# Optimization experiments

Measured on AMD Instinct MI355X. Metric: run time of the kernel, lower is better.

Reference implementation:

```python
import jax, jax.numpy as jnp
import numpy as np

N_NODES = 20000
N_GRAPH = 256
NODE_DIM = 128
MULS = (128, 64, 32)       # node irreps: 128x0e + 64x1o + 32x2e
HC = 32                    # hidden channels per irrep
HIDDEN_DIM = 64
N_PATH = 9                 # feasible uuw paths into 0e+1e+2e
W_NUMEL = N_PATH * HC * HC # 9216


def _tables():
    # real Clebsch-Gordan tensors built from cartesian tensor algebra,
    # normalized so that sum(C**2) = 2*l_out + 1 (component normalization)
    eps = np.zeros((3, 3, 3))
    eps[0, 1, 2] = eps[1, 2, 0] = eps[2, 0, 1] = 1.0
    eps[0, 2, 1] = eps[2, 1, 0] = eps[1, 0, 2] = -1.0
    s2, s6 = 1 / np.sqrt(2), 1 / np.sqrt(6)
    Q2 = np.zeros((5, 3, 3))  # orthonormal basis of traceless symmetric 3x3
    Q2[0, 0, 1] = Q2[0, 1, 0] = s2          # xy
    Q2[1, 1, 2] = Q2[1, 2, 1] = s2          # yz
    Q2[2, 0, 0] = Q2[2, 1, 1] = -s6; Q2[2, 2, 2] = 2 * s6  # z2
    Q2[3, 0, 2] = Q2[3, 2, 0] = s2          # xz
    Q2[4, 0, 0] = s2; Q2[4, 1, 1] = -s2     # x2-y2

    def nrm(C, l3):
        return C * np.sqrt((2 * l3 + 1) / (C ** 2).sum())

    C000 = np.ones((1, 1, 1))
    C022 = np.eye(5)[None, :, :]
    C110 = np.eye(3).reshape(3, 3, 1) / np.sqrt(3)
    C111 = eps / np.sqrt(2)
    C112 = np.transpose(Q2, (1, 2, 0))
    C202 = np.eye(5)[:, None, :]
    C220 = np.eye(5).reshape(5, 5, 1) / np.sqrt(5)
    M = np.einsum('iab,jdb->ijad', Q2, Q2)  # [5,5,3,3]
    C221 = nrm(np.einsum('cad,ijad->ijc', eps, M), 1)
    S = 0.5 * (M + np.transpose(M, (0, 1, 3, 2)))
    S = S - np.trace(S, axis1=2, axis2=3)[..., None, None] * np.eye(3) / 3.0
    C222 = nrm(np.einsum('kad,ijad->ijk', Q2, S), 2)
    # sph2cart change of basis: 9 spherical comps (0e+1e+2e) -> 3x3 cartesian
    Qc = np.zeros((3, 3, 9))
    Qc[:, :, 0] = np.eye(3) / np.sqrt(3)        # isotropic part
    Qc[:, :, 1:4] = eps / np.sqrt(2)            # antisymmetric part
    Qc[:, :, 4:9] = np.transpose(Q2, (1, 2, 0)) # symmetric traceless part
    return [C000, C022, C110, C111, C112, C202, C220, C221, C222], Qc

_CGS, _QC = _tables()


def setup_inputs() -> dict:
    key = jax.random.key(0)
    ks = jax.random.split(key, 12)
    f32 = jnp.float32
    d_sph = MULS[0] + 3 * MULS[1] + 5 * MULS[2]  # 480
    return {
        'x_scalar': jax.random.normal(ks[0], (N_NODES, NODE_DIM), f32),
        'x_spherical': jax.random.normal(ks[1], (N_NODES, d_sph), f32),
        'batch': jnp.sort(jax.random.randint(ks[2], (N_NODES,), 0, N_GRAPH)),
        'W0e': jax.random.normal(ks[3], (MULS[0], HC), f32),
        'W1o': jax.random.normal(ks[4], (MULS[1], HC), f32),
        'W2e': jax.random.normal(ks[5], (MULS[2], HC), f32),
        'Wm1': jax.random.normal(ks[6], (NODE_DIM, HIDDEN_DIM), f32) / np.sqrt(NODE_DIM),
        'bm1': jnp.zeros((HIDDEN_DIM,), f32),
        'Wm2': jax.random.normal(ks[7], (HIDDEN_DIM, W_NUMEL), f32) / np.sqrt(HIDDEN_DIM),
        'bm2': jnp.zeros((W_NUMEL,), f32),
        'P0': jax.random.normal(ks[8], (3 * HC,), f32),
        'P1': jax.random.normal(ks[9], (2 * HC,), f32),
        'P2': jax.random.normal(ks[10], (4 * HC,), f32),
    }


def reference(x_scalar, x_spherical, batch, W0e, W1o, W2e, Wm1, bm1, Wm2, bm2, P0, P1, P2):
    n = x_scalar.shape[0]
    m0, m1, m2 = MULS
    # split node features into irrep blocks
    x0 = x_spherical[:, :m0, None]                        # [N,128,1] 0e
    x1 = x_spherical[:, m0:m0 + 3 * m1].reshape(n, m1, 3) # [N,64,3]  1o
    x2 = x_spherical[:, m0 + 3 * m1:].reshape(n, m2, 5)   # [N,32,5]  2e
    # pre_lin: per-irrep channel mixing (e3nn-style 1/sqrt(fan_in))
    h = [jnp.einsum('num,uv->nvm', x, W) / np.sqrt(W.shape[0])
         for x, W in ((x0, W0e), (x1, W1o), (x2, W2e))]   # each [N,32,2l+1]
    # per-node tensor-product weights from scalar features
    w = (jax.nn.silu(x_scalar @ Wm1 + bm1) @ Wm2 + bm2).reshape(n, N_PATH, HC, HC)
    # uuw tensor product, path order matches _CGS
    paths = ((0, 0), (0, 2), (1, 1), (1, 1), (1, 1), (2, 0), (2, 2), (2, 2), (2, 2))
    inv_u = 1.0 / np.sqrt(HC)
    outs = []
    for k, (i, j) in enumerate(paths):
        C = jnp.asarray(_CGS[k], x_scalar.dtype)
        outs.append(jnp.einsum('pqr,nup,nuq,nuw->nwr', C, h[i], h[j], w[:, k]) * inv_u)
    # post_lin: combine paths of each output l into a single channel
    y0 = jnp.einsum('num,u->nm', jnp.concatenate([outs[0], outs[2], outs[6]], 1), P0) / np.sqrt(3 * HC)
    y1 = jnp.einsum('num,u->nm', jnp.concatenate([outs[3], outs[7]], 1), P1) / np.sqrt(2 * HC)
    y2 = jnp.einsum('num,u->nm', jnp.concatenate([outs[1], outs[4], outs[5], outs[8]], 1), P2) / np.sqrt(4 * HC)
    sph = jnp.concatenate([y0, y1, y2], axis=1)           # [N,9]
    cart = jnp.einsum('abi,ni->nab', jnp.asarray(_QC, sph.dtype), sph)  # [N,3,3]
    red = jax.ops.segment_sum(cart, batch, num_segments=N_GRAPH)        # [B,3,3]
    # if_trace is False (if_iso=False): roll every non-batch dim by 1
    return jnp.roll(jnp.roll(red, 1, axis=1), 1, axis=2)
```

## Files before the change

kernel.cpp:

```cpp
#include <hip/hip_runtime.h>
#include <math.h>

#define OFF_W2P 0
#define OFF_B2P 12288
#define WS_FLOATS 12480

#define SC_Y0 0.0180421959121758f
#define SC_Y2 0.015625f
#define S2f 0.70710678118654752f
#define S6f 0.40824829046386302f
#define TWOS2f 1.41421356237309505f
#define TWOS6f 0.81649658092772603f
#define ISQRT3 0.57735026918962576f
#define ISQRT5 0.44721359549995794f
#define H0SC 0.08838834764831845f
#define H1SC 0.125f
#define H2SC 0.17677669529663689f

__device__ static inline float dot32(const float* __restrict__ a,
                                     const float* __restrict__ b) {
  const float4* a4 = (const float4*)a;
  const float4* b4 = (const float4*)b;
  float acc = 0.f;
#pragma unroll
  for (int q = 0; q < 8; ++q) {
    float4 x = a4[q], y = b4[q];
    acc += x.x * y.x + x.y * y.y + x.z * y.z + x.w * y.w;
  }
  return acc;
}

__global__ __launch_bounds__(256) void prep_kernel(
    const float* __restrict__ Wm2, const float* __restrict__ bm2,
    const float* __restrict__ P0, const float* __restrict__ P2,
    float* __restrict__ ws, float* __restrict__ out) {
  int j = blockIdx.x * 256 + threadIdx.x;
  if (j < 2304) out[j] = 0.f;

  if (j < 12288) {
    const int c = j / 192, o = j % 192;
    const int s = o >> 5, u = o & 31;
    int k; const float* P; float sc;
    switch (s) {
      case 0: k = 0; P = P0;      sc = SC_Y0; break;
      case 1: k = 1; P = P2;      sc = SC_Y2; break;
      case 2: k = 2; P = P0 + 32; sc = SC_Y0; break;
      case 3: k = 4; P = P2 + 32; sc = SC_Y2; break;
      case 4: k = 6; P = P0 + 64; sc = SC_Y0; break;
      default: k = 8; P = P2 + 96; sc = SC_Y2; break;
    }
    float acc = dot32(Wm2 + c * 9216 + k * 1024 + u * 32, P);
    if (s == 1) acc += dot32(Wm2 + c * 9216 + 5 * 1024 + u * 32, P2 + 64);
    ws[OFF_W2P + j] = acc * sc;
  } else if (j < 12480) {
    const int o = j - 12288;
    const int s = o >> 5, u = o & 31;
    int k; const float* P; float sc;
    switch (s) {
      case 0: k = 0; P = P0;      sc = SC_Y0; break;
      case 1: k = 1; P = P2;      sc = SC_Y2; break;
      case 2: k = 2; P = P0 + 32; sc = SC_Y0; break;
      case 3: k = 4; P = P2 + 32; sc = SC_Y2; break;
      case 4: k = 6; P = P0 + 64; sc = SC_Y0; break;
      default: k = 8; P = P2 + 96; sc = SC_Y2; break;
    }
    float acc = dot32(bm2 + k * 1024 + u * 32, P);
    if (s == 1) acc += dot32(bm2 + 5 * 1024 + u * 32, P2 + 64);
    ws[OFF_B2P + o] = acc * sc;
  }
}

__global__ __launch_bounds__(256, 4) void fused_kernel(
    const float* __restrict__ xs_g, const float* __restrict__ xsph,
    const float* __restrict__ W0e, const float* __restrict__ W1o,
    const float* __restrict__ W2e,
    const float* __restrict__ Wm1, const float* __restrict__ bm1,
    const float* __restrict__ ws, const int* __restrict__ batch,
    float* __restrict__ out, const float norm2) {
  __shared__ __align__(16) float smem[9312];
  float (*xp)[512] = (float (*)[512])smem;
  float (*Vt)[192] = (float (*)[192])smem;
  float (*hi2)[64] = (float (*)[64])(smem + 8192);
  float (*sphs)[6] = (float (*)[6])(smem + 9216);

  const int tid = threadIdx.x;
  const int n0 = blockIdx.x * 16;

  float4 st[7];
  float4 st7;
#pragma unroll
  for (int k = 0; k < 7; ++k) {
    const int d = tid + k * 256;
    const int r = d / 120, c = d % 120;
    st[k] = *(const float4*)(xsph + (size_t)(n0 + r) * 480 + c * 4);
  }
  if (tid < 128) {
    const int d = tid + 1792;
    const int r = d / 120, c = d % 120;
    st7 = *(const float4*)(xsph + (size_t)(n0 + r) * 480 + c * 4);
  }

  {
    const int n = tid >> 4, c0 = (tid & 15) * 4;
    const float* xr = xs_g + (size_t)(n0 + n) * 128;
    float a0 = 0.f, a1 = 0.f, a2 = 0.f, a3 = 0.f;
#pragma unroll 4
    for (int mq = 0; mq < 32; ++mq) {
      const float4 xv = *(const float4*)(xr + mq * 4);
      const float4 w0 = *(const float4*)(Wm1 + (mq * 4 + 0) * 64 + c0);
      const float4 w1 = *(const float4*)(Wm1 + (mq * 4 + 1) * 64 + c0);
      const float4 w2 = *(const float4*)(Wm1 + (mq * 4 + 2) * 64 + c0);
      const float4 w3 = *(const float4*)(Wm1 + (mq * 4 + 3) * 64 + c0);
      a0 += xv.x * w0.x + xv.y * w1.x + xv.z * w2.x + xv.w * w3.x;
      a1 += xv.x * w0.y + xv.y * w1.y + xv.z * w2.y + xv.w * w3.y;
      a2 += xv.x * w0.z + xv.y * w1.z + xv.z * w2.z + xv.w * w3.z;
      a3 += xv.x * w0.w + xv.y * w1.w + xv.z * w2.w + xv.w * w3.w;
    }
    const float4 bb = *(const float4*)(bm1 + c0);
    const float z0 = a0 + bb.x, z1 = a1 + bb.y, z2 = a2 + bb.z, z3 = a3 + bb.w;
    float4 s;
    s.x = z0 / (1.f + __expf(-z0));
    s.y = z1 / (1.f + __expf(-z1));
    s.z = z2 / (1.f + __expf(-z2));
    s.w = z3 / (1.f + __expf(-z3));
    *(float4*)&hi2[n][c0] = s;
  }

#pragma unroll
  for (int k = 0; k < 7; ++k) {
    const int d = tid + k * 256;
    const int r = d / 120, c = d % 120;
    *(float4*)&xp[r][c * 4] = st[k];
  }
  if (tid < 128) {
    const int d = tid + 1792;
    const int r = d / 120, c = d % 120;
    *(float4*)&xp[r][c * 4] = st7;
  }
  __syncthreads();

  const int u = tid & 31, ni = tid >> 5;
  const float* rowA = xp[ni];
  const float* rowB = xp[ni + 8];

  float h0A, h0B;
  {
    float aA = 0.f, aB = 0.f;
#pragma unroll 4
    for (int mq = 0; mq < 32; ++mq) {
      const float4 xa = *(const float4*)(rowA + mq * 4);
      const float4 xb = *(const float4*)(rowB + mq * 4);
      const float w0 = W0e[(mq * 4 + 0) * 32 + u];
      const float w1 = W0e[(mq * 4 + 1) * 32 + u];
      const float w2 = W0e[(mq * 4 + 2) * 32 + u];
      const float w3 = W0e[(mq * 4 + 3) * 32 + u];
      aA += xa.x * w0 + xa.y * w1 + xa.z * w2 + xa.w * w3;
      aB += xb.x * w0 + xb.y * w1 + xb.z * w2 + xb.w * w3;
    }
    h0A = aA * H0SC; h0B = aB * H0SC;
  }

  float h1A[3], h1B[3];
  {
    float aA[3] = {0.f, 0.f, 0.f}, aB[3] = {0.f, 0.f, 0.f};
#pragma unroll 2
    for (int mq = 0; mq < 16; ++mq) {
      const float4 a0 = *(const float4*)(rowA + 128 + mq * 12);
      const float4 a1 = *(const float4*)(rowA + 128 + mq * 12 + 4);
      const float4 a2 = *(const float4*)(rowA + 128 + mq * 12 + 8);
      const float4 b0 = *(const float4*)(rowB + 128 + mq * 12);
      const float4 b1 = *(const float4*)(rowB + 128 + mq * 12 + 4);
      const float4 b2 = *(const float4*)(rowB + 128 + mq * 12 + 8);
      const float xa[12] = {a0.x, a0.y, a0.z, a0.w, a1.x, a1.y, a1.z, a1.w,
                            a2.x, a2.y, a2.z, a2.w};
      const float xb[12] = {b0.x, b0.y, b0.z, b0.w, b1.x, b1.y, b1.z, b1.w,
                            b2.x, b2.y, b2.z, b2.w};
#pragma unroll
      for (int mm = 0; mm < 4; ++mm) {
        const float w = W1o[(mq * 4 + mm) * 32 + u];
#pragma unroll
        for (int j = 0; j < 3; ++j) {
          aA[j] += xa[mm * 3 + j] * w;
          aB[j] += xb[mm * 3 + j] * w;
        }
      }
    }
#pragma unroll
    for (int j = 0; j < 3; ++j) { h1A[j] = aA[j] * H1SC; h1B[j] = aB[j] * H1SC; }
  }

  float h2A[5], h2B[5];
  {
    float aA[5] = {0.f, 0.f, 0.f, 0.f, 0.f}, aB[5] = {0.f, 0.f, 0.f, 0.f, 0.f};
#pragma unroll 2
    for (int mq = 0; mq < 8; ++mq) {
      const float4 a0 = *(const float4*)(rowA + 320 + mq * 20);
      const float4 a1 = *(const float4*)(rowA + 320 + mq * 20 + 4);
      const float4 a2 = *(const float4*)(rowA + 320 + mq * 20 + 8);
      const float4 a3 = *(const float4*)(rowA + 320 + mq * 20 + 12);
      const float4 a4 = *(const float4*)(rowA + 320 + mq * 20 + 16);
      const float4 b0 = *(const float4*)(rowB + 320 + mq * 20);
      const float4 b1 = *(const float4*)(rowB + 320 + mq * 20 + 4);
      const float4 b2 = *(const float4*)(rowB + 320 + mq * 20 + 8);
      const float4 b3 = *(const float4*)(rowB + 320 + mq * 20 + 12);
      const float4 b4 = *(const float4*)(rowB + 320 + mq * 20 + 16);
      const float xa[20] = {a0.x, a0.y, a0.z, a0.w, a1.x, a1.y, a1.z, a1.w,
                            a2.x, a2.y, a2.z, a2.w, a3.x, a3.y, a3.z, a3.w,
                            a4.x, a4.y, a4.z, a4.w};
      const float xb[20] = {b0.x, b0.y, b0.z, b0.w, b1.x, b1.y, b1.z, b1.w,
                            b2.x, b2.y, b2.z, b2.w, b3.x, b3.y, b3.z, b3.w,
                            b4.x, b4.y, b4.z, b4.w};
#pragma unroll
      for (int mm = 0; mm < 4; ++mm) {
        const float w = W2e[(mq * 4 + mm) * 32 + u];
#pragma unroll
        for (int j = 0; j < 5; ++j) {
          aA[j] += xa[mm * 5 + j] * w;
          aB[j] += xb[mm * 5 + j] * w;
        }
      }
    }
#pragma unroll
    for (int j = 0; j < 5; ++j) { h2A[j] = aA[j] * H2SC; h2B[j] = aB[j] * H2SC; }
  }
  __syncthreads();

  if (tid < 192) {
    const int o = tid;
    float acc[16];
    {
      const float b = ws[OFF_B2P + o];
#pragma unroll
      for (int n = 0; n < 16; ++n) acc[n] = b;
    }
    for (int c4 = 0; c4 < 64; c4 += 4) {
      const float w0 = ws[OFF_W2P + (c4 + 0) * 192 + o];
      const float w1 = ws[OFF_W2P + (c4 + 1) * 192 + o];
      const float w2 = ws[OFF_W2P + (c4 + 2) * 192 + o];
      const float w3 = ws[OFF_W2P + (c4 + 3) * 192 + o];
#pragma unroll
      for (int n = 0; n < 16; ++n) {
        const float4 h = *(const float4*)&hi2[n][c4];
        acc[n] += h.x * w0 + h.y * w1 + h.z * w2 + h.w * w3;
      }
    }
#pragma unroll
    for (int n = 0; n < 16; ++n) Vt[n][o] = acc[n];
  }
  __syncthreads();

#pragma unroll
  for (int it = 0; it < 2; ++it) {
    const int ln = ni + 8 * it;
    const float h0 = (it == 0) ? h0A : h0B;
    const float h1a = (it == 0) ? h1A[0] : h1B[0];
    const float h1b = (it == 0) ? h1A[1] : h1B[1];
    const float h1c = (it == 0) ? h1A[2] : h1B[2];
    float h2v[5];
#pragma unroll
    for (int j = 0; j < 5; ++j) h2v[j] = (it == 0) ? h2A[j] : h2B[j];

    const float* Vp = &Vt[ln][u];
    const float v0 = Vp[0], v15 = Vp[32], v2 = Vp[64], v3 = Vp[96];
    const float v5 = Vp[128], v6 = Vp[160];

    const float d11 = h1a * h1a + h1b * h1b + h1c * h1c;
    const float d22 = h2v[0] * h2v[0] + h2v[1] * h2v[1] + h2v[2] * h2v[2] +
                      h2v[3] * h2v[3] + h2v[4] * h2v[4];
    float y0 = v0 * h0 * h0 + v2 * d11 * ISQRT3 + v5 * d22 * ISQRT5;

    const float o00 = h1a * h1a, o01 = h1a * h1b, o02 = h1a * h1c;
    const float o11 = h1b * h1b, o12 = h1b * h1c, o22 = h1c * h1c;
    const float t40 = TWOS2f * o01, t41 = TWOS2f * o12;
    const float t42 = S6f * (2.f * o22 - o00 - o11);
    const float t43 = TWOS2f * o02, t44 = S2f * (o00 - o11);

    const float A00 = -S6f * h2v[2] + S2f * h2v[4];
    const float A01 = S2f * h2v[0];
    const float A02 = S2f * h2v[3];
    const float A11 = -S6f * h2v[2] - S2f * h2v[4];
    const float A12 = S2f * h2v[1];
    const float A22 = TWOS6f * h2v[2];
    const float B00 = A00 * A00 + A01 * A01 + A02 * A02;
    const float B01 = A00 * A01 + A01 * A11 + A02 * A12;
    const float B02 = A00 * A02 + A01 * A12 + A02 * A22;
    const float B11 = A01 * A01 + A11 * A11 + A12 * A12;
    const float B12 = A01 * A02 + A11 * A12 + A12 * A22;
    const float B22 = A02 * A02 + A12 * A12 + A22 * A22;
    const float t80 = TWOS2f * B01, t81 = TWOS2f * B12;
    const float t82 = S6f * (2.f * B22 - B00 - B11);
    const float t83 = TWOS2f * B02, t84 = S2f * (B00 - B11);

    const float w15 = v15 * h0;
    const float v6n = v6 * norm2;
    float y2r[5];
    y2r[0] = w15 * h2v[0] + v3 * t40 + v6n * t80;
    y2r[1] = w15 * h2v[1] + v3 * t41 + v6n * t81;
    y2r[2] = w15 * h2v[2] + v3 * t42 + v6n * t82;
    y2r[3] = w15 * h2v[3] + v3 * t43 + v6n * t83;
    y2r[4] = w15 * h2v[4] + v3 * t44 + v6n * t84;

#pragma unroll
    for (int off = 16; off > 0; off >>= 1) {
      y0 += __shfl_xor(y0, off, 32);
#pragma unroll
      for (int r = 0; r < 5; ++r) y2r[r] += __shfl_xor(y2r[r], off, 32);
    }

    if (u == 0) {
      sphs[ln][0] = y0;
#pragma unroll
      for (int r = 0; r < 5; ++r) sphs[ln][1 + r] = y2r[r];
    }
  }
  __syncthreads();

  if (tid < 9) {
    const float QW[9][6] = {
        {ISQRT3, 0.f, 0.f, -S6f, 0.f, S2f},
        {0.f, S2f, 0.f, 0.f, 0.f, 0.f},
        {0.f, 0.f, 0.f, 0.f, S2f, 0.f},
        {0.f, S2f, 0.f, 0.f, 0.f, 0.f},
        {ISQRT3, 0.f, 0.f, -S6f, 0.f, -S2f},
        {0.f, 0.f, S2f, 0.f, 0.f, 0.f},
        {0.f, 0.f, 0.f, 0.f, S2f, 0.f},
        {0.f, 0.f, S2f, 0.f, 0.f, 0.f},
        {ISQRT3, 0.f, 0.f, TWOS6f, 0.f, 0.f}};
    const int a = tid / 3, b = tid % 3;
    const int rolled = ((a + 1) % 3) * 3 + ((b + 1) % 3);
    const float c0 = QW[tid][0], c1 = QW[tid][1], c2 = QW[tid][2];
    const float c3 = QW[tid][3], c4 = QW[tid][4], c5 = QW[tid][5];
    int cur_g = batch[n0];
    float acc = 0.f;
#pragma unroll
    for (int q = 0; q < 16; ++q) {
      const int g = batch[n0 + q];
      const float val = c0 * sphs[q][0] + c1 * sphs[q][1] + c2 * sphs[q][2] +
                        c3 * sphs[q][3] + c4 * sphs[q][4] + c5 * sphs[q][5];
      if (g != cur_g) {
        atomicAdd(out + cur_g * 9 + rolled, acc);
        acc = 0.f;
        cur_g = g;
      }
      acc += val;
    }
    atomicAdd(out + cur_g * 9 + rolled, acc);
  }
}

extern "C" void kernel_launch(void* const* d_in, const int* in_sizes, int n_in,
                              void* d_out, int out_size, void* d_ws, size_t ws_size,
                              hipStream_t stream) {
  const float* x_scalar = (const float*)d_in[0];
  const float* x_sph    = (const float*)d_in[1];
  const int*   batch    = (const int*)d_in[2];
  const float* W0e      = (const float*)d_in[3];
  const float* W1o      = (const float*)d_in[4];
  const float* W2e      = (const float*)d_in[5];
  const float* Wm1      = (const float*)d_in[6];
  const float* bm1      = (const float*)d_in[7];
  const float* Wm2      = (const float*)d_in[8];
  const float* bm2      = (const float*)d_in[9];
  const float* P0       = (const float*)d_in[10];
  const float* P2       = (const float*)d_in[12];
  float* ws  = (float*)d_ws;
  float* out = (float*)d_out;

  if (ws_size < (size_t)WS_FLOATS * sizeof(float)) return;

  double Q2[5][3][3] = {};
  const double s2d = 0.70710678118654752440, s6d = 0.40824829046386301637;
  Q2[0][0][1] = Q2[0][1][0] = s2d;
  Q2[1][1][2] = Q2[1][2][1] = s2d;
  Q2[2][0][0] = Q2[2][1][1] = -s6d; Q2[2][2][2] = 2.0 * s6d;
  Q2[3][0][2] = Q2[3][2][0] = s2d;
  Q2[4][0][0] = s2d; Q2[4][1][1] = -s2d;
  double ss = 0.0;
  for (int i = 0; i < 5; ++i)
    for (int jj = 0; jj < 5; ++jj) {
      double S[3][3];
      for (int a = 0; a < 3; ++a)
        for (int d = 0; d < 3; ++d) {
          double m1 = 0, m2 = 0;
          for (int b = 0; b < 3; ++b) {
            m1 += Q2[i][a][b] * Q2[jj][d][b];
            m2 += Q2[i][d][b] * Q2[jj][a][b];
          }
          S[a][d] = 0.5 * (m1 + m2);
        }
      double tr = (S[0][0] + S[1][1] + S[2][2]) / 3.0;
      S[0][0] -= tr; S[1][1] -= tr; S[2][2] -= tr;
      for (int kk = 0; kk < 5; ++kk) {
        double cc = 0;
        for (int a = 0; a < 3; ++a)
          for (int d = 0; d < 3; ++d) cc += Q2[kk][a][d] * S[a][d];
        ss += cc * cc;
      }
    }
  const float norm2 = (float)sqrt(5.0 / ss);

  prep_kernel<<<49, 256, 0, stream>>>(Wm2, bm2, P0, P2, ws, out);
  fused_kernel<<<1250, 256, 0, stream>>>(x_scalar, x_sph, W0e, W1o, W2e,
                                         Wm1, bm1, ws, batch, out, norm2);
}
```

Baseline: 153.0 us.

## Split warps between equivariant projections and path-weight GEMM to run concurrently

Threads 0-127 now compute the irrep projections with each thread handling one node and four channels via float4 weight loads. Threads 128-255 compute the hidden-to-path GEMM at the same time into a separate padded Vt buffer. This removes one barrier and the serialization between the two phases. Each thread now reduces over its four channels before a shorter 8-lane shuffle. The cost is a larger shared-memory footprint, which lowers the launch-bounds occupancy hint from 4 to 3, plus more registers per thread and some divergence in the GEMM half.

```diff
diff --git a/kernel.cpp b/kernel.cpp
--- a/kernel.cpp
+++ b/kernel.cpp
@@ -16,6 +16,8 @@
 #define H0SC 0.08838834764831845f
 #define H1SC 0.125f
 #define H2SC 0.17677669529663689f
+
+#define COMP(v, q) ((q) == 0 ? (v).x : (q) == 1 ? (v).y : (q) == 2 ? (v).z : (v).w)
 
 __device__ static inline float dot32(const float* __restrict__ a,
                                      const float* __restrict__ b) {
@@ -70,18 +72,18 @@
   }
 }
 
-__global__ __launch_bounds__(256, 4) void fused_kernel(
+__global__ __launch_bounds__(256, 3) void fused_kernel(
     const float* __restrict__ xs_g, const float* __restrict__ xsph,
     const float* __restrict__ W0e, const float* __restrict__ W1o,
     const float* __restrict__ W2e,
     const float* __restrict__ Wm1, const float* __restrict__ bm1,
     const float* __restrict__ ws, const int* __restrict__ batch,
     float* __restrict__ out, const float norm2) {
-  __shared__ __align__(16) float smem[9312];
-  float (*xp)[512] = (float (*)[512])smem;
-  float (*Vt)[192] = (float (*)[192])smem;
-  float (*hi2)[64] = (float (*)[64])(smem + 8192);
-  float (*sphs)[6] = (float (*)[6])(smem + 9216);
+  __shared__ __align__(16) float smem[11952];
+  float (*xp)[484] = (float (*)[484])smem;
+  float (*hi2)[64] = (float (*)[64])(smem + 7744);
+  float (*Vt)[193] = (float (*)[193])(smem + 8768);
+  float (*sphs)[6] = (float (*)[6])(smem + 11856);
 
   const int tid = threadIdx.x;
   const int n0 = blockIdx.x * 16;
@@ -139,178 +141,175 @@
   }
   __syncthreads();
 
-  const int u = tid & 31, ni = tid >> 5;
-  const float* rowA = xp[ni];
-  const float* rowB = xp[ni + 8];
-
-  float h0A, h0B;
-  {
-    float aA = 0.f, aB = 0.f;
+  const int n = tid >> 3, ug = tid & 7, u0 = ug * 4;
+  float4 acc0 = {0.f, 0.f, 0.f, 0.f};
+  float4 acc1[3];
+  float4 acc2[5];
+
+  if (tid < 128) {
+    const float* row = xp[n];
 #pragma unroll 4
     for (int mq = 0; mq < 32; ++mq) {
-      const float4 xa = *(const float4*)(rowA + mq * 4);
-      const float4 xb = *(const float4*)(rowB + mq * 4);
-      const float w0 = W0e[(mq * 4 + 0) * 32 + u];
-      const float w1 = W0e[(mq * 4 + 1) * 32 + u];
-      const float w2 = W0e[(mq * 4 + 2) * 32 + u];
-      const float w3 = W0e[(mq * 4 + 3) * 32 + u];
-      aA += xa.x * w0 + xa.y * w1 + xa.z * w2 + xa.w * w3;
-      aB += xb.x * w0 + xb.y * w1 + xb.z * w2 + xb.w * w3;
-    }
-    h0A = aA * H0SC; h0B = aB * H0SC;
-  }
-
-  float h1A[3], h1B[3];
-  {
-    float aA[3] = {0.f, 0.f, 0.f}, aB[3] = {0.f, 0.f, 0.f};
+      const float4 xv = *(const float4*)(row + mq * 4);
+#pragma unroll
+      for (int r = 0; r < 4; ++r) {
+        const float4 w = *(const float4*)(W0e + (mq * 4 + r) * 32 + u0);
+        const float xr = COMP(xv, r);
+        acc0.x += xr * w.x; acc0.y += xr * w.y;
+        acc0.z += xr * w.z; acc0.w += xr * w.w;
+      }
+    }
+#pragma unroll
+    for (int j = 0; j < 3; ++j) acc1[j] = make_float4(0.f, 0.f, 0.f, 0.f);
 #pragma unroll 2
     for (int mq = 0; mq < 16; ++mq) {
-      const float4 a0 = *(const float4*)(rowA + 128 + mq * 12);
-      const float4 a1 = *(const float4*)(rowA + 128 + mq * 12 + 4);
-      const float4 a2 = *(const float4*)(rowA + 128 + mq * 12 + 8);
-      const float4 b0 = *(const float4*)(rowB + 128 + mq * 12);
-      const float4 b1 = *(const float4*)(rowB + 128 + mq * 12 + 4);
-      const float4 b2 = *(const float4*)(rowB + 128 + mq * 12 + 8);
-      const float xa[12] = {a0.x, a0.y, a0.z, a0.w, a1.x, a1.y, a1.z, a1.w,
-                            a2.x, a2.y, a2.z, a2.w};
-      const float xb[12] = {b0.x, b0.y, b0.z, b0.w, b1.x, b1.y, b1.z, b1.w,
+      const float4 b0 = *(const float4*)(row + 128 + mq * 12);
+      const float4 b1 = *(const float4*)(row + 128 + mq * 12 + 4);
+      const float4 b2 = *(const float4*)(row + 128 + mq * 12 + 8);
+      const float xa[12] = {b0.x, b0.y, b0.z, b0.w, b1.x, b1.y, b1.z, b1.w,
                             b2.x, b2.y, b2.z, b2.w};
 #pragma unroll
       for (int mm = 0; mm < 4; ++mm) {
-        const float w = W1o[(mq * 4 + mm) * 32 + u];
+        const float4 w = *(const float4*)(W1o + (mq * 4 + mm) * 32 + u0);
 #pragma unroll
         for (int j = 0; j < 3; ++j) {
-          aA[j] += xa[mm * 3 + j] * w;
-          aB[j] += xb[mm * 3 + j] * w;
+          const float xr = xa[mm * 3 + j];
+          acc1[j].x += xr * w.x; acc1[j].y += xr * w.y;
+          acc1[j].z += xr * w.z; acc1[j].w += xr * w.w;
         }
       }
     }
 #pragma unroll
-    for (int j = 0; j < 3; ++j) { h1A[j] = aA[j] * H1SC; h1B[j] = aB[j] * H1SC; }
-  }
-
-  float h2A[5], h2B[5];
-  {
-    float aA[5] = {0.f, 0.f, 0.f, 0.f, 0.f}, aB[5] = {0.f, 0.f, 0.f, 0.f, 0.f};
+    for (int j = 0; j < 5; ++j) acc2[j] = make_float4(0.f, 0.f, 0.f, 0.f);
 #pragma unroll 2
     for (int mq = 0; mq < 8; ++mq) {
-      const float4 a0 = *(const float4*)(rowA + 320 + mq * 20);
-      const float4 a1 = *(const float4*)(rowA + 320 + mq * 20 + 4);
-      const float4 a2 = *(const float4*)(rowA + 320 + mq * 20 + 8);
-      const float4 a3 = *(const float4*)(rowA + 320 + mq * 20 + 12);
-      const float4 a4 = *(const float4*)(rowA + 320 + mq * 20 + 16);
-      const float4 b0 = *(const float4*)(rowB + 320 + mq * 20);
-      const float4 b1 = *(const float4*)(rowB + 320 + mq * 20 + 4);
-      const float4 b2 = *(const float4*)(rowB + 320 + mq * 20 + 8);
-      const float4 b3 = *(const float4*)(rowB + 320 + mq * 20 + 12);
-      const float4 b4 = *(const float4*)(rowB + 320 + mq * 20 + 16);
-      const float xa[20] = {a0.x, a0.y, a0.z, a0.w, a1.x, a1.y, a1.z, a1.w,
-                            a2.x, a2.y, a2.z, a2.w, a3.x, a3.y, a3.z, a3.w,
-                            a4.x, a4.y, a4.z, a4.w};
-      const float xb[20] = {b0.x, b0.y, b0.z, b0.w, b1.x, b1.y, b1.z, b1.w,
-                            b2.x, b2.y, b2.z, b2.w, b3.x, b3.y, b3.z, b3.w,
-                            b4.x, b4.y, b4.z, b4.w};
+      const float4 c0v = *(const float4*)(row + 320 + mq * 20);
+      const float4 c1v = *(const float4*)(row + 320 + mq * 20 + 4);
+      const float4 c2v = *(const float4*)(row + 320 + mq * 20 + 8);
+      const float4 c3v = *(const float4*)(row + 320 + mq * 20 + 12);
+      const float4 c4v = *(const float4*)(row + 320 + mq * 20 + 16);
+      const float xa[20] = {c0v.x, c0v.y, c0v.z, c0v.w, c1v.x, c1v.y, c1v.z, c1v.w,
+                            c2v.x, c2v.y, c2v.z, c2v.w, c3v.x, c3v.y, c3v.z, c3v.w,
+                            c4v.x, c4v.y, c4v.z, c4v.w};
 #pragma unroll
       for (int mm = 0; mm < 4; ++mm) {
-        const float w = W2e[(mq * 4 + mm) * 32 + u];
+        const float4 w = *(const float4*)(W2e + (mq * 4 + mm) * 32 + u0);
 #pragma unroll
         for (int j = 0; j < 5; ++j) {
-          aA[j] += xa[mm * 5 + j] * w;
-          aB[j] += xb[mm * 5 + j] * w;
+          const float xr = xa[mm * 5 + j];
+          acc2[j].x += xr * w.x; acc2[j].y += xr * w.y;
+          acc2[j].z += xr * w.z; acc2[j].w += xr * w.w;
         }
       }
     }
-#pragma unroll
-    for (int j = 0; j < 5; ++j) { h2A[j] = aA[j] * H2SC; h2B[j] = aB[j] * H2SC; }
+  } else {
+    const int j = tid - 128;
+    const bool two = (j < 64);
+    const int o2 = j + 128;
+    float accA[16], accB[16];
+    {
+      const float bA = ws[OFF_B2P + j];
+#pragma unroll
+      for (int nn = 0; nn < 16; ++nn) accA[nn] = bA;
+    }
+    if (two) {
+      const float bB = ws[OFF_B2P + o2];
+#pragma unroll
+      for (int nn = 0; nn < 16; ++nn) accB[nn] = bB;
+    }
+    for (int c4 = 0; c4 < 64; c4 += 4) {
+      const float wA0 = ws[OFF_W2P + (c4 + 0) * 192 + j];
+      const float wA1 = ws[OFF_W2P + (c4 + 1) * 192 + j];
+      const float wA2 = ws[OFF_W2P + (c4 + 2) * 192 + j];
+      const float wA3 = ws[OFF_W2P + (c4 + 3) * 192 + j];
+      float wB0, wB1, wB2, wB3;
+      if (two) {
+        wB0 = ws[OFF_W2P + (c4 + 0) * 192 + o2];
+        wB1 = ws[OFF_W2P + (c4 + 1) * 192 + o2];
+        wB2 = ws[OFF_W2P + (c4 + 2) * 192 + o2];
+        wB3 = ws[OFF_W2P + (c4 + 3) * 192 + o2];
+      }
+#pragma unroll
+      for (int nn = 0; nn < 16; ++nn) {
+        const float4 h = *(const float4*)&hi2[nn][c4];
+        accA[nn] += h.x * wA0 + h.y * wA1 + h.z * wA2 + h.w * wA3;
+        if (two) accB[nn] += h.x * wB0 + h.y * wB1 + h.z * wB2 + h.w * wB3;
+      }
+    }
+#pragma unroll
+    for (int nn = 0; nn < 16; ++nn) {
+      Vt[nn][j] = accA[nn];
+      if (two) Vt[nn][o2] = accB[nn];
+    }
   }
   __syncthreads();
 
-  if (tid < 192) {
-    const int o = tid;
-    float acc[16];
-    {
-      const float b = ws[OFF_B2P + o];
-#pragma unroll
-      for (int n = 0; n < 16; ++n) acc[n] = b;
-    }
-    for (int c4 = 0; c4 < 64; c4 += 4) {
-      const float w0 = ws[OFF_W2P + (c4 + 0) * 192 + o];
-      const float w1 = ws[OFF_W2P + (c4 + 1) * 192 + o];
-      const float w2 = ws[OFF_W2P + (c4 + 2) * 192 + o];
-      const float w3 = ws[OFF_W2P + (c4 + 3) * 192 + o];
-#pragma unroll
-      for (int n = 0; n < 16; ++n) {
-        const float4 h = *(const float4*)&hi2[n][c4];
-        acc[n] += h.x * w0 + h.y * w1 + h.z * w2 + h.w * w3;
-      }
-    }
-#pragma unroll
-    for (int n = 0; n < 16; ++n) Vt[n][o] = acc[n];
-  }
-  __syncthreads();
-
-#pragma unroll
-  for (int it = 0; it < 2; ++it) {
-    const int ln = ni + 8 * it;
-    const float h0 = (it == 0) ? h0A : h0B;
-    const float h1a = (it == 0) ? h1A[0] : h1B[0];
-    const float h1b = (it == 0) ? h1A[1] : h1B[1];
-    const float h1c = (it == 0) ? h1A[2] : h1B[2];
-    float h2v[5];
-#pragma unroll
-    for (int j = 0; j < 5; ++j) h2v[j] = (it == 0) ? h2A[j] : h2B[j];
-
-    const float* Vp = &Vt[ln][u];
-    const float v0 = Vp[0], v15 = Vp[32], v2 = Vp[64], v3 = Vp[96];
-    const float v5 = Vp[128], v6 = Vp[160];
-
-    const float d11 = h1a * h1a + h1b * h1b + h1c * h1c;
-    const float d22 = h2v[0] * h2v[0] + h2v[1] * h2v[1] + h2v[2] * h2v[2] +
-                      h2v[3] * h2v[3] + h2v[4] * h2v[4];
-    float y0 = v0 * h0 * h0 + v2 * d11 * ISQRT3 + v5 * d22 * ISQRT5;
-
-    const float o00 = h1a * h1a, o01 = h1a * h1b, o02 = h1a * h1c;
-    const float o11 = h1b * h1b, o12 = h1b * h1c, o22 = h1c * h1c;
-    const float t40 = TWOS2f * o01, t41 = TWOS2f * o12;
-    const float t42 = S6f * (2.f * o22 - o00 - o11);
-    const float t43 = TWOS2f * o02, t44 = S2f * (o00 - o11);
-
-    const float A00 = -S6f * h2v[2] + S2f * h2v[4];
-    const float A01 = S2f * h2v[0];
-    const float A02 = S2f * h2v[3];
-    const float A11 = -S6f * h2v[2] - S2f * h2v[4];
-    const float A12 = S2f * h2v[1];
-    const float A22 = TWOS6f * h2v[2];
-    const float B00 = A00 * A00 + A01 * A01 + A02 * A02;
-    const float B01 = A00 * A01 + A01 * A11 + A02 * A12;
-    const float B02 = A00 * A02 + A01 * A12 + A02 * A22;
-    const float B11 = A01 * A01 + A11 * A11 + A12 * A12;
-    const float B12 = A01 * A02 + A11 * A12 + A12 * A22;
-    const float B22 = A02 * A02 + A12 * A12 + A22 * A22;
-    const float t80 = TWOS2f * B01, t81 = TWOS2f * B12;
-    const float t82 = S6f * (2.f * B22 - B00 - B11);
-    const float t83 = TWOS2f * B02, t84 = S2f * (B00 - B11);
-
-    const float w15 = v15 * h0;
-    const float v6n = v6 * norm2;
-    float y2r[5];
-    y2r[0] = w15 * h2v[0] + v3 * t40 + v6n * t80;
-    y2r[1] = w15 * h2v[1] + v3 * t41 + v6n * t81;
-    y2r[2] = w15 * h2v[2] + v3 * t42 + v6n * t82;
-    y2r[3] = w15 * h2v[3] + v3 * t43 + v6n * t83;
-    y2r[4] = w15 * h2v[4] + v3 * t44 + v6n * t84;
-
-#pragma unroll
-    for (int off = 16; off > 0; off >>= 1) {
-      y0 += __shfl_xor(y0, off, 32);
-#pragma unroll
-      for (int r = 0; r < 5; ++r) y2r[r] += __shfl_xor(y2r[r], off, 32);
-    }
-
-    if (u == 0) {
-      sphs[ln][0] = y0;
-#pragma unroll
-      for (int r = 0; r < 5; ++r) sphs[ln][1 + r] = y2r[r];
+  if (tid < 128) {
+    float y0s = 0.f;
+    float y2s[5] = {0.f, 0.f, 0.f, 0.f, 0.f};
+#pragma unroll
+    for (int q = 0; q < 4; ++q) {
+      const int u = u0 + q;
+      const float* Vp = &Vt[n][u];
+      const float v0 = Vp[0], v15 = Vp[32], v2 = Vp[64], v3 = Vp[96];
+      const float v5 = Vp[128], v6 = Vp[160];
+
+      const float h0 = COMP(acc0, q) * H0SC;
+      const float h1a = COMP(acc1[0], q) * H1SC;
+      const float h1b = COMP(acc1[1], q) * H1SC;
+      const float h1c = COMP(acc1[2], q) * H1SC;
+      float h2v[5];
+#pragma unroll
+      for (int jj = 0; jj < 5; ++jj) h2v[jj] = COMP(acc2[jj], q) * H2SC;
+
+      const float d11 = h1a * h1a + h1b * h1b + h1c * h1c;
+      const float d22 = h2v[0] * h2v[0] + h2v[1] * h2v[1] + h2v[2] * h2v[2] +
+                        h2v[3] * h2v[3] + h2v[4] * h2v[4];
+      float y0 = v0 * h0 * h0 + v2 * d11 * ISQRT3 + v5 * d22 * ISQRT5;
+
+      const float o00 = h1a * h1a, o01 = h1a * h1b, o02 = h1a * h1c;
+      const float o11 = h1b * h1b, o12 = h1b * h1c, o22 = h1c * h1c;
+      const float t40 = TWOS2f * o01, t41 = TWOS2f * o12;
+      const float t42 = S6f * (2.f * o22 - o00 - o11);
+      const float t43 = TWOS2f * o02, t44 = S2f * (o00 - o11);
+
+      const float A00 = -S6f * h2v[2] + S2f * h2v[4];
+      const float A01 = S2f * h2v[0];
+      const float A02 = S2f * h2v[3];
+      const float A11 = -S6f * h2v[2] - S2f * h2v[4];
+      const float A12 = S2f * h2v[1];
+      const float A22 = TWOS6f * h2v[2];
+      const float B00 = A00 * A00 + A01 * A01 + A02 * A02;
+      const float B01 = A00 * A01 + A01 * A11 + A02 * A12;
+      const float B02 = A00 * A02 + A01 * A12 + A02 * A22;
+      const float B11 = A01 * A01 + A11 * A11 + A12 * A12;
+      const float B12 = A01 * A02 + A11 * A12 + A12 * A22;
+      const float B22 = A02 * A02 + A12 * A12 + A22 * A22;
+      const float t80 = TWOS2f * B01, t81 = TWOS2f * B12;
+      const float t82 = S6f * (2.f * B22 - B00 - B11);
+      const float t83 = TWOS2f * B02, t84 = S2f * (B00 - B11);
+
+      const float w15 = v15 * h0;
+      const float v6n = v6 * norm2;
+      y0s += y0;
+      y2s[0] += w15 * h2v[0] + v3 * t40 + v6n * t80;
+      y2s[1] += w15 * h2v[1] + v3 * t41 + v6n * t81;
+      y2s[2] += w15 * h2v[2] + v3 * t42 + v6n * t82;
+      y2s[3] += w15 * h2v[3] + v3 * t43 + v6n * t83;
+      y2s[4] += w15 * h2v[4] + v3 * t44 + v6n * t84;
+    }
+
+#pragma unroll
+    for (int off = 4; off > 0; off >>= 1) {
+      y0s += __shfl_xor(y0s, off, 8);
+#pragma unroll
+      for (int r = 0; r < 5; ++r) y2s[r] += __shfl_xor(y2s[r], off, 8);
+    }
+
+    if (ug == 0) {
+      sphs[n][0] = y0s;
+#pragma unroll
+      for (int r = 0; r < 5; ++r) sphs[n][1 + r] = y2s[r];
     }
   }
   __syncthreads();
```

Measured after the change: 158.8 us. +3.7%, slower.
